# Kernel optimization log

Hardware: AMD Instinct MI355X
Metric: run time of the kernel (lower is better)

The kernel has to match this reference:

```python
import math
import jax, jax.numpy as jnp
import numpy as np

B, C_IN, C_OUT, K, STYLE, H, W = 16, 512, 512, 3, 512, 64, 64


def setup_inputs() -> dict:
    key = jax.random.key(0)
    k1, k2, k3, k4 = jax.random.split(key, 4)
    return {
        "x": jax.random.normal(k1, (B, C_IN, H, W), jnp.float32),
        "style": jax.random.normal(k2, (B, STYLE), jnp.float32),
        "weight": jax.random.normal(k3, (C_OUT, C_IN, K, K), jnp.float32),  # learned conv weight (leading 1 dim of torch param squeezed)
        "mod_w": jax.random.normal(k4, (C_IN, STYLE), jnp.float32),         # EqualLinear weight
        "mod_b": jnp.ones((C_IN,), jnp.float32),                             # EqualLinear bias (bias_init=1)
    }


def reference(x, style, weight, mod_w, mod_b):
    # EqualLinear modulation: scale = 1/sqrt(style_dim), lr_mul = 1
    mod_scale = 1.0 / math.sqrt(STYLE)
    s = style @ (mod_w.T * mod_scale) + mod_b            # [B, C_IN]

    # per-sample modulated weight
    w_scale = 1.0 / math.sqrt(C_IN * K * K)
    w = w_scale * weight[None] * s[:, None, :, None, None]  # [B, C_OUT, C_IN, K, K]

    # demodulate
    demod = jax.lax.rsqrt(jnp.sum(w * w, axis=(2, 3, 4)) + 1e-8)  # [B, C_OUT]
    w = w * demod[:, :, None, None, None]

    pad = K // 2

    def conv_one(xi, wi):
        # xi: [C_IN, H, W], wi: [C_OUT, C_IN, K, K]
        return jax.lax.conv_general_dilated(
            xi[None], wi, window_strides=(1, 1),
            padding=[(pad, pad), (pad, pad)],
            dimension_numbers=("NCHW", "OIHW", "NCHW"),
        )[0]

    return jax.vmap(conv_one)(x, w)  # [B, C_OUT, H, W]
```

## Files before the change

### kernel.cpp

```cpp
#include <hip/hip_runtime.h>
#include <hip/hip_bf16.h>
#include <math.h>
#include <stdint.h>

#define B_     16
#define CI_    512
#define CO_    512
#define HH     64
#define WW     64
#define STYLE_ 512

typedef __bf16 bf16x8 __attribute__((ext_vector_type(8)));
typedef float f32x16 __attribute__((ext_vector_type(16)));

__device__ __forceinline__ int fsl(int r, int h) {
    return (2 * r + (h ^ ((r >> 2) & 1))) ^ (((r >> 4) & 1) << 1);
}

#define WS_S     0
#define WS_DEMOD 32768
#define WS_WSQ   65536
#define WS_WB    1114112
#define WS_XS    5832704

__device__ __forceinline__ void gload16(const void* g, void* l) {
    __builtin_amdgcn_global_load_lds((const __attribute__((address_space(1))) uint32_t*)g,
                                     (__attribute__((address_space(3))) uint32_t*)l, 16, 0, 0);
}

__global__ __launch_bounds__(256) void k_style2(const float* __restrict__ style,
                                                const float* __restrict__ mod_w,
                                                const float* __restrict__ mod_b,
                                                float* __restrict__ s_out) {
    const int ci   = blockIdx.x * 4 + (threadIdx.x >> 6);
    const int b    = blockIdx.y;
    const int lane = threadIdx.x & 63;
    const float4* mw = (const float4*)(mod_w + (size_t)ci * STYLE_);
    const float4* st = (const float4*)(style + (size_t)b * STYLE_);
    float acc = 0.f;
    #pragma unroll
    for (int i = 0; i < 2; ++i) {
        float4 a = mw[lane + i * 64], s = st[lane + i * 64];
        acc += a.x * s.x + a.y * s.y + a.z * s.z + a.w * s.w;
    }
    #pragma unroll
    for (int off = 32; off >= 1; off >>= 1) acc += __shfl_xor(acc, off);
    if (lane == 0)
        s_out[b * CI_ + ci] = acc * 0.044194173824159216f + mod_b[ci];
}

__global__ __launch_bounds__(256) void k_wprep(const float* __restrict__ weight,
                                               float* __restrict__ wsq, __bf16* __restrict__ wb) {
    int p = blockIdx.x * 256 + threadIdx.x;
    int co = p >> 9, ci = p & 511;
    const float* wp = weight + (size_t)p * 9;
    const int gs = ((co >> 6) << 7) + fsl(co & 63, (ci >> 3) & 1);
    float acc = 0.f;
    #pragma unroll
    for (int t = 0; t < 9; ++t) {
        float v = wp[t];
        acc += v * v;
        wb[(((size_t)(ci >> 4) * 9 + t) * 8192) + gs * 8 + (ci & 7)] = (__bf16)v;
    }
    wsq[(size_t)ci * CO_ + co] = acc;
}

__global__ __launch_bounds__(64) void k_demod(const float* __restrict__ s,
                                              const float* __restrict__ wsq,
                                              float* __restrict__ demod) {
    int b = blockIdx.x, co = blockIdx.y * 64 + threadIdx.x;
    const float w_scale2 = 1.0f / 4608.0f;
    float acc = 0.f;
    const float* sb = s + b * CI_;
    #pragma unroll 8
    for (int ci = 0; ci < CI_; ++ci) { float sv = sb[ci]; acc += sv * sv * wsq[(size_t)ci * CO_ + co]; }
    demod[b * CO_ + co] = 1.0f / sqrtf(acc * w_scale2 + 1e-8f);
}

__global__ __launch_bounds__(256) void k_xs(const float* __restrict__ x, const float* __restrict__ s,
                                            __bf16* __restrict__ xs) {
    __shared__ float Lt[64][65];
    const int y = blockIdx.x, b = blockIdx.y;
    const int tid = threadIdx.x;
    const float w_scale = 0.014731391274719739f;
    for (int ci0 = 0; ci0 < CI_; ci0 += 64) {
        for (int i = tid; i < 64 * 16; i += 256) {
            int ci = i >> 4, x4 = (i & 15) * 4;
            const float4 v = *(const float4*)&x[((size_t)(b * CI_ + ci0 + ci) * HH + y) * WW + x4];
            float sc = s[b * CI_ + ci0 + ci] * w_scale;
            Lt[ci][x4]     = v.x * sc;
            Lt[ci][x4 + 1] = v.y * sc;
            Lt[ci][x4 + 2] = v.z * sc;
            Lt[ci][x4 + 3] = v.w * sc;
        }
        __syncthreads();
        #pragma unroll
        for (int it = 0; it < 2; ++it) {
            int o = tid + it * 256;
            int xx = o & 63, oct = o >> 6;
            int cb = ci0 + oct * 8;
            int chunk = cb >> 4;
            int pp = fsl(xx + 1, oct & 1) - 2;
            bf16x8 v;
            #pragma unroll
            for (int j = 0; j < 8; ++j) v[j] = (__bf16)Lt[oct * 8 + j][xx];
            size_t idx = (((size_t)chunk * 16 + b) * 66 + (y + 1)) * 1024 + pp * 8;
            *(bf16x8*)&xs[idx] = v;
        }
        __syncthreads();
    }
    if (y == 0 || y == 63) {
        const int row = (y == 0) ? 0 : 65;
        uint32_t* xs32 = (uint32_t*)xs;
        for (int c = 0; c < 32; ++c)
            for (int i = tid; i < 512; i += 256)
                xs32[(((size_t)c * 16 + b) * 66 + row) * 512 + i] = 0;
    }
}

#define XBUF 21120
#define WBUF 18432

__global__ __launch_bounds__(256, 2) void k_conv(
    const __bf16* __restrict__ xs, const __bf16* __restrict__ wb,
    const float* __restrict__ demod, float* __restrict__ out)
{
    __shared__ __align__(128) char smem[2 * XBUF + 2 * WBUF];

    const int tid  = threadIdx.x;
    const int lane = tid & 63;
    const int wave = tid >> 6;

    const int bid  = blockIdx.x;
    const int r8   = bid & 7;
    const int q    = bid >> 3;
    const int co0  = (q & 7) * 64;
    const int tt   = q >> 3;
    const int y0   = (tt & 7) * 8;
    const int b    = r8 * 2 + (tt >> 3);
    const int pbit = (bid ^ (bid >> 8) ^ (bid >> 9)) & 1;

    const int lm = lane & 31;
    const int g2 = lane >> 5;

    for (int i = tid; i < 320; i += 256) {
        int buf = i / 160, rem = i % 160;
        int rb = rem >> 4, hh = rem & 15;
        int side = hh >> 3, dw = hh & 7;
        ((uint32_t*)smem)[buf * (XBUF / 4) + rb * 528 + side * 520 + dw] = 0;
    }
    asm volatile("s_waitcnt lgkmcnt(0)" ::: "memory");

    uint32_t soff[10];
    uint32_t sdst[10];
    if (wave < 2) {
        #pragma unroll
        for (int i = 0; i < 10; ++i) {
            int j = wave * 10 + i, rb = j >> 1, seg = j & 1;
            soff[i] = (uint32_t)((y0 + rb) * 1024 + seg * 512 + lane * 8);
            sdst[i] = (uint32_t)(rb * 2112 + 32 + seg * 1024 + lane * 16);
        }
    } else {
        #pragma unroll
        for (int i = 0; i < 9; ++i) {
            int j = (wave - 2) * 9 + i;
            int tap = j >> 1, seg = j & 1;
            soff[i] = (uint32_t)(tap * 8192 + co0 * 16 + seg * 512 + lane * 8);
            sdst[i] = (uint32_t)(j * 1024 + lane * 16);
        }
        soff[9] = 0; sdst[9] = 0;
    }

    const uint32_t acol = (uint32_t)(16 * fsl(lm, g2));
    uint32_t cbase[3];
    #pragma unroll
    for (int kw = 0; kw < 3; ++kw) cbase[kw] = (uint32_t)(16 * fsl(lm + kw, g2));
    uint32_t rbase[4];
    #pragma unroll
    for (int rr = 0; rr < 4; ++rr) rbase[rr] = (uint32_t)((2 * wave + rr) * 2112);

    f32x16 acc[2][4];
    #pragma unroll
    for (int mi = 0; mi < 2; ++mi)
        #pragma unroll
        for (int n = 0; n < 4; ++n)
            #pragma unroll
            for (int r = 0; r < 16; ++r) acc[mi][n][r] = 0.f;

    auto stage = [&](int chunk, int sel) {
        if (wave < 2) {
            const __bf16* base = xs + (size_t)chunk * 1081344 + (size_t)b * 67584;
            #pragma unroll
            for (int i = 0; i < 10; ++i) gload16(base + soff[i], smem + sel * XBUF + sdst[i]);
        } else {
            const __bf16* base = wb + (size_t)chunk * 73728;
            #pragma unroll
            for (int i = 0; i < 9; ++i) gload16(base + soff[i], smem + 2 * XBUF + sel * WBUF + sdst[i]);
        }
    };

    stage(0, 0);

#define MAIN_LOOP(PHI, PLO)                                                        \
    for (int t = 0; t < 32; ++t) {                                                 \
        if (t < 31) {                                                              \
            stage(t + 1, (t + 1) & 1);                                             \
            if (wave < 2) asm volatile("s_waitcnt vmcnt(10)" ::: "memory");        \
            else          asm volatile("s_waitcnt vmcnt(9)"  ::: "memory");        \
        } else {                                                                   \
            asm volatile("s_waitcnt vmcnt(0)" ::: "memory");                       \
        }                                                                          \
        __builtin_amdgcn_s_barrier();                                              \
        const char* xbuf = smem + (t & 1) * XBUF;                                  \
        const char* wbuf = smem + 2 * XBUF + (t & 1) * WBUF + acol;                \
        _Pragma("unroll")                                                          \
        for (int kw = 0; kw < 3; ++kw) {                                           \
            bf16x8 fa[3][2], fb[4][2];                                             \
            _Pragma("unroll")                                                      \
            for (int kh = 0; kh < 3; ++kh) {                                       \
                const char* wp = wbuf + (kh * 3 + kw) * 2048;                      \
                fa[kh][0] = *(const bf16x8*)(wp);                                  \
                fa[kh][1] = *(const bf16x8*)(wp + 1024);                           \
            }                                                                      \
            _Pragma("unroll")                                                      \
            for (int rr = 0; rr < 4; ++rr) {                                       \
                fb[rr][0] = *(const bf16x8*)(xbuf + rbase[rr] + cbase[kw]);        \
                fb[rr][1] = *(const bf16x8*)(xbuf + rbase[rr] + cbase[kw] + 1024); \
            }                                                                      \
            __builtin_amdgcn_s_setprio(PHI);                                       \
            _Pragma("unroll")                                                      \
            for (int kh = 0; kh < 3; ++kh)                                         \
                _Pragma("unroll")                                                  \
                for (int ys = 0; ys < 2; ++ys)                                     \
                    _Pragma("unroll")                                              \
                    for (int nt = 0; nt < 2; ++nt) {                               \
                        acc[0][ys * 2 + nt] = __builtin_amdgcn_mfma_f32_32x32x16_bf16( \
                            fa[kh][0], fb[ys + kh][nt], acc[0][ys * 2 + nt], 0, 0, 0); \
                        acc[1][ys * 2 + nt] = __builtin_amdgcn_mfma_f32_32x32x16_bf16( \
                            fa[kh][1], fb[ys + kh][nt], acc[1][ys * 2 + nt], 0, 0, 0); \
                    }                                                              \
            __builtin_amdgcn_s_setprio(PLO);                                       \
        }                                                                          \
        __builtin_amdgcn_s_barrier();                                              \
    }

    if (pbit) { __builtin_amdgcn_s_setprio(2); MAIN_LOOP(3, 2) }
    else      {                                MAIN_LOOP(1, 0) }
    __builtin_amdgcn_s_setprio(0);
#undef MAIN_LOOP

    #pragma unroll
    for (int mi = 0; mi < 2; ++mi) {
        #pragma unroll
        for (int ys = 0; ys < 2; ++ys) {
            const int y = y0 + 2 * wave + ys;
            float* outb = out + ((size_t)b * CO_ + co0 + mi * 32) * 4096 + (size_t)y * 64;
            #pragma unroll
            for (int reg = 0; reg < 16; ++reg) {
                const int cosub = (reg & 3) + 8 * (reg >> 2) + 4 * g2;
                const float dm = demod[b * CO_ + co0 + mi * 32 + cosub];
                outb[(size_t)cosub * 4096 + lm]      = acc[mi][ys * 2 + 0][reg] * dm;
                outb[(size_t)cosub * 4096 + 32 + lm] = acc[mi][ys * 2 + 1][reg] * dm;
            }
        }
    }
}

extern "C" void kernel_launch(void* const* d_in, const int* in_sizes, int n_in,
                              void* d_out, int out_size, void* d_ws, size_t ws_size,
                              hipStream_t stream) {
    const float* x      = (const float*)d_in[0];
    const float* style  = (const float*)d_in[1];
    const float* weight = (const float*)d_in[2];
    const float* mod_w  = (const float*)d_in[3];
    const float* mod_b  = (const float*)d_in[4];
    float* out = (float*)d_out;

    char* wsb = (char*)d_ws;
    float*  s_buf = (float*)(wsb + WS_S);
    float*  demod = (float*)(wsb + WS_DEMOD);
    float*  wsq   = (float*)(wsb + WS_WSQ);
    __bf16* wb    = (__bf16*)(wsb + WS_WB);
    __bf16* xs    = (__bf16*)(wsb + WS_XS);

    k_style2<<<dim3(CI_ / 4, B_), dim3(256), 0, stream>>>(style, mod_w, mod_b, s_buf);
    k_wprep<<<dim3(CO_ * CI_ / 256), dim3(256), 0, stream>>>(weight, wsq, wb);
    k_demod<<<dim3(B_, CO_ / 64), dim3(64), 0, stream>>>(s_buf, wsq, demod);
    k_xs<<<dim3(HH, B_), dim3(256), 0, stream>>>(x, s_buf, xs);
    k_conv<<<dim3(1024), dim3(256), 0, stream>>>(xs, wb, demod, out);
}
```

Baseline: 332.2 us.

## Load activation fragments directly from global and stage only weights in LDS

The prep kernel now writes activations into a plain padded layout: 1056 bf16 per row, with zeroed left and right halo pixels and no swizzle. The conv kernel drops the LDS double buffer for activations. Each wave reads its B-operand fragments straight from global memory into registers, and the three kw shifts become simple byte offsets. Only the weights stay double-buffered in LDS via global_load_lds. This frees LDS and removes the activation staging and its barriers, but global-load latency now sits directly before the MFMAs, with little prefetch. It also drops the alternating wave-priority scheme.

```diff
diff --git a/kernel.cpp b/kernel.cpp
--- a/kernel.cpp
+++ b/kernel.cpp
@@ -22,6 +22,10 @@
 #define WS_WSQ   65536
 #define WS_WB    1114112
 #define WS_XS    5832704
+
+#define XROW  2112
+#define XB_B  139392
+#define XCHNK 2230272
 
 __device__ __forceinline__ void gload16(const void* g, void* l) {
     __builtin_amdgcn_global_load_lds((const __attribute__((address_space(1))) uint32_t*)g,
@@ -99,33 +103,37 @@
             int o = tid + it * 256;
             int xx = o & 63, oct = o >> 6;
             int cb = ci0 + oct * 8;
-            int chunk = cb >> 4;
-            int pp = fsl(xx + 1, oct & 1) - 2;
+            int chunk = cb >> 4, h = oct & 1;
             bf16x8 v;
             #pragma unroll
             for (int j = 0; j < 8; ++j) v[j] = (__bf16)Lt[oct * 8 + j][xx];
-            size_t idx = (((size_t)chunk * 16 + b) * 66 + (y + 1)) * 1024 + pp * 8;
+            size_t idx = (((size_t)chunk * 16 + b) * 66 + (y + 1)) * 1056 + (xx + 1) * 16 + h * 8;
             *(bf16x8*)&xs[idx] = v;
         }
         __syncthreads();
+    }
+    for (int i = tid; i < 64; i += 256) {
+        int chunk = i >> 1, side = i & 1;
+        __bf16* p = xs + (((size_t)chunk * 16 + b) * 66 + (y + 1)) * 1056 + side * 1040;
+        *(bf16x8*)p = (bf16x8)(__bf16)0.0f;
+        *(bf16x8*)(p + 8) = (bf16x8)(__bf16)0.0f;
     }
     if (y == 0 || y == 63) {
         const int row = (y == 0) ? 0 : 65;
         uint32_t* xs32 = (uint32_t*)xs;
         for (int c = 0; c < 32; ++c)
-            for (int i = tid; i < 512; i += 256)
-                xs32[(((size_t)c * 16 + b) * 66 + row) * 512 + i] = 0;
-    }
-}
-
-#define XBUF 21120
+            for (int i = tid; i < 528; i += 256)
+                xs32[((((size_t)c * 16 + b) * 66 + row) * 1056) / 2 + i] = 0;
+    }
+}
+
 #define WBUF 18432
 
 __global__ __launch_bounds__(256, 2) void k_conv(
     const __bf16* __restrict__ xs, const __bf16* __restrict__ wb,
     const float* __restrict__ demod, float* __restrict__ out)
 {
-    __shared__ __align__(128) char smem[2 * XBUF + 2 * WBUF];
+    __shared__ __align__(128) char smem[2 * WBUF];
 
     const int tid  = threadIdx.x;
     const int lane = tid & 63;
@@ -138,46 +146,28 @@
     const int tt   = q >> 3;
     const int y0   = (tt & 7) * 8;
     const int b    = r8 * 2 + (tt >> 3);
-    const int pbit = (bid ^ (bid >> 8) ^ (bid >> 9)) & 1;
 
     const int lm = lane & 31;
     const int g2 = lane >> 5;
 
-    for (int i = tid; i < 320; i += 256) {
-        int buf = i / 160, rem = i % 160;
-        int rb = rem >> 4, hh = rem & 15;
-        int side = hh >> 3, dw = hh & 7;
-        ((uint32_t*)smem)[buf * (XBUF / 4) + rb * 528 + side * 520 + dw] = 0;
-    }
-    asm volatile("s_waitcnt lgkmcnt(0)" ::: "memory");
-
-    uint32_t soff[10];
-    uint32_t sdst[10];
-    if (wave < 2) {
-        #pragma unroll
-        for (int i = 0; i < 10; ++i) {
-            int j = wave * 10 + i, rb = j >> 1, seg = j & 1;
-            soff[i] = (uint32_t)((y0 + rb) * 1024 + seg * 512 + lane * 8);
-            sdst[i] = (uint32_t)(rb * 2112 + 32 + seg * 1024 + lane * 16);
-        }
-    } else {
+    const int sbase = (wave & 1) * 9;
+    auto stageW = [&](int chunk, int sel) {
+        const __bf16* base = wb + (size_t)chunk * 73728 + co0 * 16;
+        char* ldsb = smem + sel * WBUF;
         #pragma unroll
         for (int i = 0; i < 9; ++i) {
-            int j = (wave - 2) * 9 + i;
-            int tap = j >> 1, seg = j & 1;
-            soff[i] = (uint32_t)(tap * 8192 + co0 * 16 + seg * 512 + lane * 8);
-            sdst[i] = (uint32_t)(j * 1024 + lane * 16);
-        }
-        soff[9] = 0; sdst[9] = 0;
-    }
+            int sseg = sbase + i;
+            gload16(base + (sseg >> 1) * 8192 + (sseg & 1) * 512 + lane * 8,
+                    ldsb + sseg * 1024 + lane * 16);
+        }
+    };
+
+    uint32_t boff[4];
+    #pragma unroll
+    for (int rr = 0; rr < 4; ++rr)
+        boff[rr] = (uint32_t)((y0 + 2 * wave + rr) * XROW + lm * 32 + g2 * 16);
 
     const uint32_t acol = (uint32_t)(16 * fsl(lm, g2));
-    uint32_t cbase[3];
-    #pragma unroll
-    for (int kw = 0; kw < 3; ++kw) cbase[kw] = (uint32_t)(16 * fsl(lm + kw, g2));
-    uint32_t rbase[4];
-    #pragma unroll
-    for (int rr = 0; rr < 4; ++rr) rbase[rr] = (uint32_t)((2 * wave + rr) * 2112);
 
     f32x16 acc[2][4];
     #pragma unroll
@@ -187,67 +177,65 @@
             #pragma unroll
             for (int r = 0; r < 16; ++r) acc[mi][n][r] = 0.f;
 
-    auto stage = [&](int chunk, int sel) {
-        if (wave < 2) {
-            const __bf16* base = xs + (size_t)chunk * 1081344 + (size_t)b * 67584;
-            #pragma unroll
-            for (int i = 0; i < 10; ++i) gload16(base + soff[i], smem + sel * XBUF + sdst[i]);
-        } else {
-            const __bf16* base = wb + (size_t)chunk * 73728;
-            #pragma unroll
-            for (int i = 0; i < 9; ++i) gload16(base + soff[i], smem + 2 * XBUF + sel * WBUF + sdst[i]);
-        }
-    };
-
-    stage(0, 0);
-
-#define MAIN_LOOP(PHI, PLO)                                                        \
-    for (int t = 0; t < 32; ++t) {                                                 \
-        if (t < 31) {                                                              \
-            stage(t + 1, (t + 1) & 1);                                             \
-            if (wave < 2) asm volatile("s_waitcnt vmcnt(10)" ::: "memory");        \
-            else          asm volatile("s_waitcnt vmcnt(9)"  ::: "memory");        \
-        } else {                                                                   \
-            asm volatile("s_waitcnt vmcnt(0)" ::: "memory");                       \
+    const char* xb = (const char*)xs + (size_t)b * XB_B;
+
+    stageW(0, 0);
+    asm volatile("s_waitcnt vmcnt(0)" ::: "memory");
+    __builtin_amdgcn_s_barrier();
+
+#define MFMA_KW(KW, FB)                                                            \
+    {                                                                              \
+        bf16x8 fa[3][2];                                                           \
+        _Pragma("unroll")                                                          \
+        for (int kh = 0; kh < 3; ++kh) {                                           \
+            const char* wp = wbuf + (kh * 3 + (KW)) * 2048;                        \
+            fa[kh][0] = *(const bf16x8*)(wp);                                      \
+            fa[kh][1] = *(const bf16x8*)(wp + 1024);                               \
         }                                                                          \
-        __builtin_amdgcn_s_barrier();                                              \
-        const char* xbuf = smem + (t & 1) * XBUF;                                  \
-        const char* wbuf = smem + 2 * XBUF + (t & 1) * WBUF + acol;                \
+        __builtin_amdgcn_s_setprio(1);                                             \
         _Pragma("unroll")                                                          \
-        for (int kw = 0; kw < 3; ++kw) {                                           \
-            bf16x8 fa[3][2], fb[4][2];                                             \
+        for (int kh = 0; kh < 3; ++kh)                                             \
             _Pragma("unroll")                                                      \
-            for (int kh = 0; kh < 3; ++kh) {                                       \
-                const char* wp = wbuf + (kh * 3 + kw) * 2048;                      \
-                fa[kh][0] = *(const bf16x8*)(wp);                                  \
-                fa[kh][1] = *(const bf16x8*)(wp + 1024);                           \
-            }                                                                      \
-            _Pragma("unroll")                                                      \
-            for (int rr = 0; rr < 4; ++rr) {                                       \
-                fb[rr][0] = *(const bf16x8*)(xbuf + rbase[rr] + cbase[kw]);        \
-                fb[rr][1] = *(const bf16x8*)(xbuf + rbase[rr] + cbase[kw] + 1024); \
-            }                                                                      \
-            __builtin_amdgcn_s_setprio(PHI);                                       \
-            _Pragma("unroll")                                                      \
-            for (int kh = 0; kh < 3; ++kh)                                         \
+            for (int ys = 0; ys < 2; ++ys)                                         \
                 _Pragma("unroll")                                                  \
-                for (int ys = 0; ys < 2; ++ys)                                     \
-                    _Pragma("unroll")                                              \
-                    for (int nt = 0; nt < 2; ++nt) {                               \
-                        acc[0][ys * 2 + nt] = __builtin_amdgcn_mfma_f32_32x32x16_bf16( \
-                            fa[kh][0], fb[ys + kh][nt], acc[0][ys * 2 + nt], 0, 0, 0); \
-                        acc[1][ys * 2 + nt] = __builtin_amdgcn_mfma_f32_32x32x16_bf16( \
-                            fa[kh][1], fb[ys + kh][nt], acc[1][ys * 2 + nt], 0, 0, 0); \
-                    }                                                              \
-            __builtin_amdgcn_s_setprio(PLO);                                       \
-        }                                                                          \
-        __builtin_amdgcn_s_barrier();                                              \
-    }
-
-    if (pbit) { __builtin_amdgcn_s_setprio(2); MAIN_LOOP(3, 2) }
-    else      {                                MAIN_LOOP(1, 0) }
-    __builtin_amdgcn_s_setprio(0);
-#undef MAIN_LOOP
+                for (int nt = 0; nt < 2; ++nt) {                                   \
+                    acc[0][ys * 2 + nt] = __builtin_amdgcn_mfma_f32_32x32x16_bf16( \
+                        fa[kh][0], FB[ys + kh][nt], acc[0][ys * 2 + nt], 0, 0, 0); \
+                    acc[1][ys * 2 + nt] = __builtin_amdgcn_mfma_f32_32x32x16_bf16( \
+                        fa[kh][1], FB[ys + kh][nt], acc[1][ys * 2 + nt], 0, 0, 0); \
+                }                                                                  \
+        __builtin_amdgcn_s_setprio(0);                                             \
+    }
+
+    for (int t = 0; t < 32; ++t) {
+        const char* xc = xb + (size_t)t * XCHNK;
+        const char* wbuf = smem + (t & 1) * WBUF + acol;
+
+        bf16x8 fb0[4][2], fb1[4][2], fb2[4][2];
+        #pragma unroll
+        for (int rr = 0; rr < 4; ++rr) {
+            fb0[rr][0] = *(const bf16x8*)(xc + boff[rr]);
+            fb0[rr][1] = *(const bf16x8*)(xc + boff[rr] + 1024);
+            fb1[rr][0] = *(const bf16x8*)(xc + boff[rr] + 32);
+            fb1[rr][1] = *(const bf16x8*)(xc + boff[rr] + 32 + 1024);
+        }
+        if (t < 31) stageW(t + 1, (t + 1) & 1);
+
+        MFMA_KW(0, fb0)
+
+        #pragma unroll
+        for (int rr = 0; rr < 4; ++rr) {
+            fb2[rr][0] = *(const bf16x8*)(xc + boff[rr] + 64);
+            fb2[rr][1] = *(const bf16x8*)(xc + boff[rr] + 64 + 1024);
+        }
+
+        MFMA_KW(1, fb1)
+        MFMA_KW(2, fb2)
+
+        asm volatile("s_waitcnt vmcnt(0)" ::: "memory");
+        __builtin_amdgcn_s_barrier();
+    }
+#undef MFMA_KW
 
     #pragma unroll
     for (int mi = 0; mi < 2; ++mi) {
```

New measurement: 401.9 us. +21.0%, slower.
